# Kernel optimization log

Hardware: AMD Instinct MI355X
Metric: run time of the kernel (lower is better)

The kernel has to match this reference:

```python
import jax, jax.numpy as jnp
import numpy as np

TEMPERATURE = 0.5
EPS = 1e-8  # F.cosine_similarity eps


def _neg_mask_indices(B):
    # mask: ones, zero diagonal, zero the two positive off-diagonals
    N = 2 * B
    mask = np.ones((N, N), dtype=bool)
    np.fill_diagonal(mask, False)
    idx = np.arange(B)
    mask[idx, idx + B] = False
    mask[idx + B, idx] = False
    rows, cols = np.nonzero(mask)  # static, computed at trace time
    return rows, cols


def setup_inputs() -> dict:
    key = jax.random.key(0)
    k1, k2 = jax.random.split(key)
    B, D = 4096, 128
    z_i = jax.random.normal(k1, (B, D), dtype=jnp.float32)
    z_j = jax.random.normal(k2, (B, D), dtype=jnp.float32)
    return {"z_i": z_i, "z_j": z_j}


def reference(z_i, z_j):
    B = z_i.shape[0]
    N = 2 * B
    z = jnp.concatenate([z_i, z_j], axis=0)  # [N, D]
    norm = jnp.maximum(jnp.linalg.norm(z, axis=1, keepdims=True), EPS)
    zn = z / norm
    sim = (zn @ zn.T) / TEMPERATURE  # [N, N] cosine similarity / temp

    # positives: the i <-> i+B pairs
    sim_i_j = jnp.diagonal(sim, offset=B)
    sim_j_i = jnp.diagonal(sim, offset=-B)
    positives = jnp.concatenate([sim_i_j, sim_j_i], axis=0)[:, None]  # [N, 1]

    rows, cols = _neg_mask_indices(B)
    negatives = sim[rows, cols].reshape(N, N - 2)  # [N, N-2]

    logits = jnp.concatenate([positives, negatives], axis=1)  # [N, N-1]
    # cross-entropy with labels == 0 (positive is column 0)
    loss = jnp.mean(jax.nn.logsumexp(logits, axis=1) - logits[:, 0])
    return loss
```

## Files before the change

### kernel.cpp

```cpp
#include <hip/hip_runtime.h>
#include <hip/hip_bf16.h>
#include <math.h>


typedef __attribute__((ext_vector_type(8))) short bf16x8;
typedef __attribute__((ext_vector_type(4))) float f32x4;

#define NROWS 8192
#define DDIM  128
#define BHALF 4096
#define CHUNK 32
#define TILE  128
#define NCG   16
#define CGSZ  512
#define NCHUNK 16
#define SQRT_E2S 1.6986435980707531f
#define LN2      0.6931471805599453f
#define EXPDIAG  7.38905609893065f

static __device__ __forceinline__ unsigned short f2bf(float f) {
  unsigned int u = __float_as_uint(f);
  unsigned int r = (u + 0x7fffu + ((u >> 16) & 1u)) >> 16;
  return (unsigned short)r;
}

static __device__ __forceinline__ void glds16(const unsigned short* g, unsigned short* l) {
  __builtin_amdgcn_global_load_lds((const __attribute__((address_space(1))) unsigned int*)g,
                                   (__attribute__((address_space(3))) unsigned int*)l,
                                   16, 0, 0);
}

__global__ void norm_kernel(const float* __restrict__ zi, const float* __restrict__ zj,
                            unsigned short* __restrict__ zn,
                            float* __restrict__ pos, float* __restrict__ out) {
  __shared__ float2 xbuf[2][64];
  int wave = threadIdx.x >> 6;
  int lane = threadIdx.x & 63;
  int pi   = blockIdx.x * 2 + (wave & 1);
  int row  = pi + (wave >> 1) * BHALF;
  const float* src = (row < BHALF) ? (zi + (size_t)row * DDIM)
                                   : (zj + (size_t)(row - BHALF) * DDIM);
  float2 v = *(const float2*)(src + 2 * lane);
  float ss = v.x * v.x + v.y * v.y;
  #pragma unroll
  for (int off = 1; off < 64; off <<= 1) ss += __shfl_xor(ss, off);
  float scale = SQRT_E2S / fmaxf(sqrtf(ss), 1e-8f);
  v.x *= scale; v.y *= scale;
  unsigned int lo = f2bf(v.x), hi = f2bf(v.y);
  ((unsigned int*)(zn + (size_t)row * DDIM))[lane] = lo | (hi << 16);

  if (wave >= 2) xbuf[wave - 2][lane] = v;
  __syncthreads();
  if (wave < 2) {
    float2 w = xbuf[wave][lane];
    float d = v.x * w.x + v.y * w.y;
    #pragma unroll
    for (int off = 1; off < 64; off <<= 1) d += __shfl_xor(d, off);
    if (lane == 0) pos[pi] = d;
  }
  if (blockIdx.x == 0 && threadIdx.x == 0) out[0] = 0.0f;
}

__global__ __launch_bounds__(256, 2)
void sim_kernel(const unsigned short* __restrict__ zn, float* __restrict__ part) {
  __shared__ unsigned short lds[4 * CHUNK * DDIM];

  const int strip = blockIdx.x >> 4;
  const int cg    = blockIdx.x & 15;
  const int wave  = threadIdx.x >> 6;
  const int lane  = threadIdx.x & 63;
  const int l15   = lane & 15;
  const int quad  = lane >> 4;

  const int row_base = strip * TILE + wave * 32;
  const int col0     = cg * CGSZ;

  bf16x8 a[2][4];
  const unsigned short* abase = zn + (size_t)(row_base + l15) * DDIM + quad * 8;
  #pragma unroll
  for (int mi = 0; mi < 2; ++mi)
    #pragma unroll
    for (int kf = 0; kf < 4; ++kf)
      a[mi][kf] = *(const bf16x8*)(abase + mi * 16 * DDIM + kf * 32);
  __builtin_amdgcn_sched_barrier(0);

  const int t0 = wave * 64 + lane;
  const int r0 = t0 >> 4,         c0 = (t0 & 15) ^ (r0 & 15);
  const int r1 = (t0 + 256) >> 4, c1 = (t0 & 15) ^ (r1 & 15);
  const unsigned short* gst0 = zn + (size_t)(col0 + r0) * DDIM + c0 * 8;
  const unsigned short* gst1 = zn + (size_t)(col0 + r1) * DDIM + c1 * 8;

  #pragma unroll
  for (int ch = 0; ch < 4; ++ch) {
    glds16(gst0 + (size_t)ch * CHUNK * DDIM, lds + ch * 4096 + wave * 512);
    glds16(gst1 + (size_t)ch * CHUNK * DDIM, lds + ch * 4096 + 2048 + wave * 512);
  }
  __builtin_amdgcn_sched_barrier(0);

  int rdoff[4];
  #pragma unroll
  for (int kf = 0; kf < 4; ++kf)
    rdoff[kf] = l15 * DDIM + (((quad + 4 * kf) ^ l15) << 3);

  float rs[2][4];
  #pragma unroll
  for (int mi = 0; mi < 2; ++mi)
    #pragma unroll
    for (int r = 0; r < 4; ++r) rs[mi][r] = 0.0f;

#define SIM_PHASE(CH, VM)                                                      \
  {                                                                            \
    asm volatile("s_waitcnt vmcnt(" VM ")" ::: "memory");                      \
    __builtin_amdgcn_s_barrier();                                              \
    __builtin_amdgcn_sched_barrier(0);                                         \
    const unsigned short* lb = lds + ((CH) & 3) * 4096;                        \
    _Pragma("unroll")                                                          \
    for (int ni = 0; ni < 2; ++ni) {                                           \
      bf16x8 b[4];                                                             \
      _Pragma("unroll")                                                        \
      for (int kf = 0; kf < 4; ++kf)                                           \
        b[kf] = *(const bf16x8*)(lb + ni * 16 * DDIM + rdoff[kf]);             \
      f32x4 acc[2];                                                            \
      _Pragma("unroll")                                                        \
      for (int mi = 0; mi < 2; ++mi) {                                         \
        f32x4 z = {0.0f, 0.0f, 0.0f, 0.0f};                                    \
        acc[mi] = __builtin_amdgcn_mfma_f32_16x16x32_bf16(a[mi][0], b[0], z, 0, 0, 0); \
      }                                                                        \
      _Pragma("unroll")                                                        \
      for (int kf = 1; kf < 4; ++kf)                                           \
        _Pragma("unroll")                                                      \
        for (int mi = 0; mi < 2; ++mi)                                         \
          acc[mi] = __builtin_amdgcn_mfma_f32_16x16x32_bf16(a[mi][kf], b[kf], acc[mi], 0, 0, 0); \
      _Pragma("unroll")                                                        \
      for (int mi = 0; mi < 2; ++mi)                                           \
        _Pragma("unroll")                                                      \
        for (int r = 0; r < 4; ++r)                                            \
          rs[mi][r] += __builtin_amdgcn_exp2f(acc[mi][r]);                     \
    }                                                                          \
    __builtin_amdgcn_sched_barrier(0);                                         \
    __builtin_amdgcn_s_barrier();                                              \
    if ((CH) + 4 < NCHUNK) {                                                   \
      glds16(gst0 + (size_t)((CH) + 4) * CHUNK * DDIM,                         \
             lds + ((CH) & 3) * 4096 + wave * 512);                            \
      glds16(gst1 + (size_t)((CH) + 4) * CHUNK * DDIM,                         \
             lds + ((CH) & 3) * 4096 + 2048 + wave * 512);                     \
    }                                                                          \
  }

  for (int ch = 0; ch < 13; ++ch)
    SIM_PHASE(ch, "6")
  SIM_PHASE(13, "4")
  SIM_PHASE(14, "2")
  SIM_PHASE(15, "0")
#undef SIM_PHASE

  #pragma unroll
  for (int mi = 0; mi < 2; ++mi)
    #pragma unroll
    for (int r = 0; r < 4; ++r) {
      float v = rs[mi][r];
      v += __shfl_xor(v, 1);
      v += __shfl_xor(v, 2);
      v += __shfl_xor(v, 4);
      v += __shfl_xor(v, 8);
      if (l15 == 0)
        part[(size_t)cg * NROWS + row_base + mi * 16 + quad * 4 + r] = v;
    }
}

__global__ void finalize_kernel(const float* __restrict__ part,
                                const float* __restrict__ pos,
                                float* __restrict__ out) {
  __shared__ float red[4];
  int r = blockIdx.x * 256 + threadIdx.x;
  float s = 0.0f;
  #pragma unroll
  for (int k = 0; k < NCG; ++k) s += part[(size_t)k * NROWS + r];
  float v = logf(s - EXPDIAG) - LN2 * pos[r & (BHALF - 1)];
  #pragma unroll
  for (int off = 1; off < 64; off <<= 1) v += __shfl_xor(v, off);
  int wave = threadIdx.x >> 6, lane = threadIdx.x & 63;
  if (lane == 0) red[wave] = v;
  __syncthreads();
  if (threadIdx.x == 0)
    atomicAdd(out, (red[0] + red[1] + red[2] + red[3]) * (1.0f / 8192.0f));
}

extern "C" void kernel_launch(void* const* d_in, const int* in_sizes, int n_in,
                              void* d_out, int out_size, void* d_ws, size_t ws_size,
                              hipStream_t stream) {
  const float* zi = (const float*)d_in[0];
  const float* zj = (const float*)d_in[1];
  char* ws = (char*)d_ws;
  unsigned short* zn = (unsigned short*)ws;
  float* part = (float*)(ws + (size_t)NROWS * DDIM * 2);
  float* pos  = (float*)(ws + (size_t)NROWS * DDIM * 2
                            + (size_t)NCG * NROWS * 4);
  float* out = (float*)d_out;

  norm_kernel<<<2048, 256, 0, stream>>>(zi, zj, zn, pos, out);
  sim_kernel<<<1024, 256, 0, stream>>>(zn, part);
  finalize_kernel<<<32, 256, 0, stream>>>(part, pos, out);
}
```

Measured before the change: 92.29 us.

## Replace LDS-staged B tiles with direct per-wave global register loads

Drops the shared-memory staging of column tiles (global_load_lds plus swizzled LDS reads and block barriers). Each wave now loads its B fragments straight from global memory into registers, double-buffered across two register sets. This removes block-level barriers and LDS traffic, but each of the four waves now fetches the same column data separately, so global/L2 traffic rises fourfold and register pressure grows.

```diff
diff --git a/kernel.cpp b/kernel.cpp
--- a/kernel.cpp
+++ b/kernel.cpp
@@ -9,8 +9,6 @@
 #define NROWS 8192
 #define DDIM  128
 #define BHALF 4096
-#define CHUNK 32
-#define TILE  128
 #define NCG   16
 #define CGSZ  512
 #define NCHUNK 16
@@ -22,12 +20,6 @@
   unsigned int u = __float_as_uint(f);
   unsigned int r = (u + 0x7fffu + ((u >> 16) & 1u)) >> 16;
   return (unsigned short)r;
-}
-
-static __device__ __forceinline__ void glds16(const unsigned short* g, unsigned short* l) {
-  __builtin_amdgcn_global_load_lds((const __attribute__((address_space(1))) unsigned int*)g,
-                                   (__attribute__((address_space(3))) unsigned int*)l,
-                                   16, 0, 0);
 }
 
 __global__ void norm_kernel(const float* __restrict__ zi, const float* __restrict__ zj,
@@ -63,16 +55,14 @@
 
 __global__ __launch_bounds__(256, 2)
 void sim_kernel(const unsigned short* __restrict__ zn, float* __restrict__ part) {
-  __shared__ unsigned short lds[4 * CHUNK * DDIM];
+  const int w    = threadIdx.x >> 6;
+  const int lane = threadIdx.x & 63;
+  const int l15  = lane & 15;
+  const int quad = lane >> 4;
 
-  const int strip = blockIdx.x >> 4;
   const int cg    = blockIdx.x & 15;
-  const int wave  = threadIdx.x >> 6;
-  const int lane  = threadIdx.x & 63;
-  const int l15   = lane & 15;
-  const int quad  = lane >> 4;
-
-  const int row_base = strip * TILE + wave * 32;
+  const int strip = (blockIdx.x >> 4) * 4 + w;
+  const int row_base = strip * 32;
   const int col0     = cg * CGSZ;
 
   bf16x8 a[2][4];
@@ -82,25 +72,6 @@
     #pragma unroll
     for (int kf = 0; kf < 4; ++kf)
       a[mi][kf] = *(const bf16x8*)(abase + mi * 16 * DDIM + kf * 32);
-  __builtin_amdgcn_sched_barrier(0);
-
-  const int t0 = wave * 64 + lane;
-  const int r0 = t0 >> 4,         c0 = (t0 & 15) ^ (r0 & 15);
-  const int r1 = (t0 + 256) >> 4, c1 = (t0 & 15) ^ (r1 & 15);
-  const unsigned short* gst0 = zn + (size_t)(col0 + r0) * DDIM + c0 * 8;
-  const unsigned short* gst1 = zn + (size_t)(col0 + r1) * DDIM + c1 * 8;
-
-  #pragma unroll
-  for (int ch = 0; ch < 4; ++ch) {
-    glds16(gst0 + (size_t)ch * CHUNK * DDIM, lds + ch * 4096 + wave * 512);
-    glds16(gst1 + (size_t)ch * CHUNK * DDIM, lds + ch * 4096 + 2048 + wave * 512);
-  }
-  __builtin_amdgcn_sched_barrier(0);
-
-  int rdoff[4];
-  #pragma unroll
-  for (int kf = 0; kf < 4; ++kf)
-    rdoff[kf] = l15 * DDIM + (((quad + 4 * kf) ^ l15) << 3);
 
   float rs[2][4];
   #pragma unroll
@@ -108,51 +79,49 @@
     #pragma unroll
     for (int r = 0; r < 4; ++r) rs[mi][r] = 0.0f;
 
-#define SIM_PHASE(CH, VM)                                                      \
+  const unsigned short* bbase = zn + (size_t)(col0 + l15) * DDIM + quad * 8;
+
+#define LOADB(B, CH)                                                           \
   {                                                                            \
-    asm volatile("s_waitcnt vmcnt(" VM ")" ::: "memory");                      \
-    __builtin_amdgcn_s_barrier();                                              \
-    __builtin_amdgcn_sched_barrier(0);                                         \
-    const unsigned short* lb = lds + ((CH) & 3) * 4096;                        \
+    const unsigned short* bp = bbase + (size_t)(CH) * 32 * DDIM;               \
     _Pragma("unroll")                                                          \
-    for (int ni = 0; ni < 2; ++ni) {                                           \
-      bf16x8 b[4];                                                             \
-      _Pragma("unroll")                                                        \
-      for (int kf = 0; kf < 4; ++kf)                                           \
-        b[kf] = *(const bf16x8*)(lb + ni * 16 * DDIM + rdoff[kf]);             \
-      f32x4 acc[2];                                                            \
-      _Pragma("unroll")                                                        \
-      for (int mi = 0; mi < 2; ++mi) {                                         \
-        f32x4 z = {0.0f, 0.0f, 0.0f, 0.0f};                                    \
-        acc[mi] = __builtin_amdgcn_mfma_f32_16x16x32_bf16(a[mi][0], b[0], z, 0, 0, 0); \
-      }                                                                        \
-      _Pragma("unroll")                                                        \
-      for (int kf = 1; kf < 4; ++kf)                                           \
-        _Pragma("unroll")                                                      \
-        for (int mi = 0; mi < 2; ++mi)                                         \
-          acc[mi] = __builtin_amdgcn_mfma_f32_16x16x32_bf16(a[mi][kf], b[kf], acc[mi], 0, 0, 0); \
-      _Pragma("unroll")                                                        \
-      for (int mi = 0; mi < 2; ++mi)                                           \
-        _Pragma("unroll")                                                      \
-        for (int r = 0; r < 4; ++r)                                            \
-          rs[mi][r] += __builtin_amdgcn_exp2f(acc[mi][r]);                     \
-    }                                                                          \
-    __builtin_amdgcn_sched_barrier(0);                                         \
-    __builtin_amdgcn_s_barrier();                                              \
-    if ((CH) + 4 < NCHUNK) {                                                   \
-      glds16(gst0 + (size_t)((CH) + 4) * CHUNK * DDIM,                         \
-             lds + ((CH) & 3) * 4096 + wave * 512);                            \
-      glds16(gst1 + (size_t)((CH) + 4) * CHUNK * DDIM,                         \
-             lds + ((CH) & 3) * 4096 + 2048 + wave * 512);                     \
+    for (int kf = 0; kf < 4; ++kf) {                                           \
+      B[0][kf] = *(const bf16x8*)(bp + kf * 32);                               \
+      B[1][kf] = *(const bf16x8*)(bp + 16 * DDIM + kf * 32);                   \
     }                                                                          \
   }
 
-  for (int ch = 0; ch < 13; ++ch)
-    SIM_PHASE(ch, "6")
-  SIM_PHASE(13, "4")
-  SIM_PHASE(14, "2")
-  SIM_PHASE(15, "0")
-#undef SIM_PHASE
+#define COMPB(B)                                                               \
+  {                                                                            \
+    _Pragma("unroll")                                                          \
+    for (int ni = 0; ni < 2; ++ni) {                                           \
+      f32x4 z = {0.0f, 0.0f, 0.0f, 0.0f};                                      \
+      f32x4 acc0 = __builtin_amdgcn_mfma_f32_16x16x32_bf16(a[0][0], B[ni][0], z, 0, 0, 0); \
+      f32x4 acc1 = __builtin_amdgcn_mfma_f32_16x16x32_bf16(a[1][0], B[ni][0], z, 0, 0, 0); \
+      _Pragma("unroll")                                                        \
+      for (int kf = 1; kf < 4; ++kf) {                                         \
+        acc0 = __builtin_amdgcn_mfma_f32_16x16x32_bf16(a[0][kf], B[ni][kf], acc0, 0, 0, 0); \
+        acc1 = __builtin_amdgcn_mfma_f32_16x16x32_bf16(a[1][kf], B[ni][kf], acc1, 0, 0, 0); \
+      }                                                                        \
+      _Pragma("unroll")                                                        \
+      for (int r = 0; r < 4; ++r) {                                            \
+        rs[0][r] += __builtin_amdgcn_exp2f(acc0[r]);                           \
+        rs[1][r] += __builtin_amdgcn_exp2f(acc1[r]);                           \
+      }                                                                        \
+    }                                                                          \
+  }
+
+  bf16x8 bA[2][4], bB[2][4];
+  LOADB(bA, 0)
+  #pragma unroll 1
+  for (int ch = 0; ch < NCHUNK; ch += 2) {
+    LOADB(bB, ch + 1)
+    COMPB(bA)
+    if (ch + 2 < NCHUNK) LOADB(bA, ch + 2)
+    COMPB(bB)
+  }
+#undef LOADB
+#undef COMPB
 
   #pragma unroll
   for (int mi = 0; mi < 2; ++mi)
```

Measured after the change: 124.7 us. 1.35x slower.
